# Performance work log

Measured on AMD Instinct MI355X. Metric: run time of the kernel, lower is better.

The kernel has to match this reference:

```python
import jax, jax.numpy as jnp
import numpy as np

B, C, H, W = 4, 128, 96, 96
INTER = C // 2


def setup_inputs() -> dict:
    key = jax.random.key(0)
    ks = jax.random.split(key, 6)
    scale = 1.0 / np.sqrt(C)
    return {
        "x1": jax.random.normal(ks[0], (B, C, H, W), dtype=jnp.float32),
        "x2": jax.random.normal(ks[1], (B, C, H, W), dtype=jnp.float32),
        "w_theta": jax.random.normal(ks[2], (INTER, C), dtype=jnp.float32) * scale,
        "w_phi": jax.random.normal(ks[3], (INTER, C), dtype=jnp.float32) * scale,
        "w_g": jax.random.normal(ks[4], (INTER, C), dtype=jnp.float32) * scale,
        "w_mask": jax.random.normal(ks[5], (C, INTER), dtype=jnp.float32) * (1.0 / np.sqrt(INTER)),
    }


def reference(x1, x2, w_theta, w_phi, w_g, w_mask):
    b, c, h1, w1 = x1.shape  # c == full channel
    inter = c // 2
    # 1x1 convs (no bias) == channel GEMMs
    theta = jnp.einsum('ic,bchw->bihw', w_theta, x1)   # [b, inter, h1, w1]
    phi   = jnp.einsum('ic,bchw->bihw', w_phi,   x2)   # [b, inter, h2, w2]
    g     = jnp.einsum('ic,bchw->bihw', w_g,     x2)   # [b, inter, h2, w2]
    # Faithful to original: .view(b, c, -1) with c = FULL channel count,
    # so the flattened length is H*W/2 and the contraction dim is c (row-major reshape).
    theta = theta.reshape(b, c, -1).transpose(0, 2, 1)  # [b, N1, c], N1 = h1*w1//2
    phi = phi.reshape(b, c, -1)                         # [b, c, N2]
    g = g.reshape(b, c, -1).transpose(0, 2, 1)          # [b, N2, c]
    scores = jnp.einsum('bnc,bcm->bnm', theta, phi)     # [b, N1, N2]
    attn = jax.nn.softmax(scores, axis=1)               # softmax over dim=1 (query axis!)
    y = jnp.einsum('bnm,bmc->bnc', attn, g)             # [b, N1, c]
    y = y.transpose(0, 2, 1).reshape(b, inter, h1, w1)  # [b, inter, h1, w1]
    mask = jnp.einsum('ci,bihw->bchw', w_mask, y)       # [b, c, h1, w1]
    return mask + x1
```

## Files before the change

kernel.cpp:

```cpp
#include <hip/hip_runtime.h>

typedef __attribute__((ext_vector_type(8))) short short8;
typedef __attribute__((ext_vector_type(4))) float f32x4;
typedef __attribute__((ext_vector_type(16))) float f32x16;
typedef unsigned short u16;
typedef unsigned int u32;

#define NB 4
#define CH 128
#define INTER2 64
#define HW2 9216
#define NN 4608
#define NSLICE 16
#define SLW2 288
#define PCH 136
#define APITCH 136

#if __has_builtin(__builtin_amdgcn_exp2f)
#define EXP2F __builtin_amdgcn_exp2f
#else
#define EXP2F exp2f
#endif

__device__ __forceinline__ u16 f2bf(float f) {
  u32 u = __float_as_uint(f);
  u += 0x7fffu + ((u >> 16) & 1u);
  return (u16)(u >> 16);
}
__device__ __forceinline__ float bf2f(u16 h) { return __uint_as_float(((u32)h) << 16); }
__device__ __forceinline__ u32 cvtpk(float lo, float hi) {
  u32 r;
  asm("v_cvt_pk_bf16_f32 %0, %1, %2" : "=v"(r) : "v"(lo), "v"(hi));
  return r;
}
__device__ __forceinline__ void gl_lds16(const u16* g, u16* l) {
  __builtin_amdgcn_global_load_lds(
      (const __attribute__((address_space(1))) unsigned int*)g,
      (__attribute__((address_space(3))) unsigned int*)l, 16, 0, 0);
}

__global__ void k_wcvt(const float* __restrict__ wt, const float* __restrict__ wp,
                       const float* __restrict__ wg, const float* __restrict__ wm,
                       u16* __restrict__ wtb, u16* __restrict__ wpb,
                       u16* __restrict__ wgb, u16* __restrict__ wmb) {
  int i = blockIdx.x * 256 + threadIdx.x;
  if (i < CH * INTER2) {
    wtb[i] = f2bf(wt[i]);
    wpb[i] = f2bf(wp[i]);
    wgb[i] = f2bf(wg[i]);
    wmb[i] = f2bf(wm[i]);
  }
}

__global__ __launch_bounds__(256) void k_conv(const float* __restrict__ x1,
                                              const float* __restrict__ x2,
                                              const u16* __restrict__ wtb,
                                              const u16* __restrict__ wpb,
                                              const u16* __restrict__ wgb,
                                              u16* __restrict__ Tt,
                                              u16* __restrict__ Pt,
                                              u16* __restrict__ Gn) {
  __shared__ u16 xT[64 * PCH];
  __shared__ u16 ot[64 * 72];
  const int tid = threadIdx.x;
  const int w = tid >> 6, l = tid & 63, lr = l & 15, lg = l >> 4;
  const int pt = blockIdx.x, b = blockIdx.y, z = blockIdx.z;
  const int p0 = pt * 64;
  const int h = (p0 >= NN) ? 1 : 0;
  const int n0 = p0 - h * NN;
  const float* X = (z ? x2 : x1) + (size_t)b * CH * HW2;

  {
    const int pq = (l & 15) * 4;
    const int cs = w + 4 * (l >> 4);
#pragma unroll
    for (int it = 0; it < 8; it++) {
      const int c = it * 16 + cs;
      float4 v = *(const float4*)(X + (size_t)c * HW2 + p0 + pq);
      xT[(pq + 0) * PCH + c] = f2bf(v.x);
      xT[(pq + 1) * PCH + c] = f2bf(v.y);
      xT[(pq + 2) * PCH + c] = f2bf(v.z);
      xT[(pq + 3) * PCH + c] = f2bf(v.w);
    }
  }
  short8 wsP[4], wsG[4];
  {
    const u16* W1 = z ? wpb : wtb;
#pragma unroll
    for (int ks = 0; ks < 4; ks++)
      wsP[ks] = *(const short8*)(W1 + (w * 16 + lr) * CH + ks * 32 + lg * 8);
    if (z) {
#pragma unroll
      for (int ks = 0; ks < 4; ks++)
        wsG[ks] = *(const short8*)(wgb + (w * 16 + lr) * CH + ks * 32 + lg * 8);
    }
  }
  __syncthreads();
  short8 xf[4][4];
#pragma unroll
  for (int tp = 0; tp < 4; tp++)
#pragma unroll
    for (int ks = 0; ks < 4; ks++)
      xf[tp][ks] = *(const short8*)(&xT[(tp * 16 + lr) * PCH + ks * 32 + lg * 8]);

  f32x4 accP[4];
#pragma unroll
  for (int tp = 0; tp < 4; tp++) {
#pragma unroll
    for (int j = 0; j < 4; j++) accP[tp][j] = 0.f;
#pragma unroll
    for (int ks = 0; ks < 4; ks++)
      accP[tp] = __builtin_amdgcn_mfma_f32_16x16x32_bf16(xf[tp][ks], wsP[ks], accP[tp], 0, 0, 0);
  }
#pragma unroll
  for (int tp = 0; tp < 4; tp++) {
#pragma unroll
    for (int j = 0; j < 4; j++)
      ot[(tp * 16 + lg * 4 + j) * 72 + w * 16 + lr] = f2bf(accP[tp][j]);
  }
  if (z) {
    f32x4 accG[4];
#pragma unroll
    for (int tp = 0; tp < 4; tp++) {
#pragma unroll
      for (int j = 0; j < 4; j++) accG[tp][j] = 0.f;
#pragma unroll
      for (int ks = 0; ks < 4; ks++)
        accG[tp] = __builtin_amdgcn_mfma_f32_16x16x32_bf16(wsG[ks], xf[tp][ks], accG[tp], 0, 0, 0);
    }
    u16* Gb = Gn + (size_t)b * CH * NN;
#pragma unroll
    for (int tp = 0; tp < 4; tp++) {
#pragma unroll
      for (int j = 0; j < 4; j++) {
        const int ig = w * 16 + lg * 4 + j;
        Gb[(size_t)((h << 6) + ig) * NN + n0 + tp * 16 + lr] = f2bf(accG[tp][j]);
      }
    }
  }
  __syncthreads();
  {
    u16* dst = (z ? Pt : Tt) + (size_t)b * NN * CH;
#pragma unroll
    for (int q = 0; q < 2; q++) {
      const int idx = tid * 2 + q;
      const int p = idx >> 3, c8 = (idx & 7) * 8;
      uint4 v = *(const uint4*)(&ot[p * 72 + c8]);
      *(uint4*)(dst + (size_t)(n0 + p) * CH + h * 64 + c8) = v;
    }
  }
}

__global__ __launch_bounds__(256) void k_den(const u16* __restrict__ Tt,
                                             const u16* __restrict__ Pt,
                                             float* __restrict__ denp) {
  const int tid = threadIdx.x;
  const int w = tid >> 6, l = tid & 63, lm = l & 31, lh = l >> 5;
  const int s = blockIdx.x & 15, mt = blockIdx.x >> 4;
  const int b = blockIdx.y;
  const int m0 = mt * 256;
  const int nbase = s * SLW2;
  const u16* PtB = Pt + (size_t)b * NN * CH;
  const u16* TtB = Tt + (size_t)b * NN * CH;

  short8 bf[2][8];
#pragma unroll
  for (int ms = 0; ms < 2; ms++)
#pragma unroll
    for (int ks = 0; ks < 8; ks++)
      bf[ms][ks] = *(const short8*)(PtB + (size_t)(m0 + w * 64 + ms * 32 + lm) * CH + ks * 16 + lh * 8);

  float den0 = 0.f, den1 = 0.f;
  short8 ac[8], an[8];
#pragma unroll
  for (int ks = 0; ks < 8; ks++)
    ac[ks] = *(const short8*)(TtB + (size_t)(nbase + lm) * CH + ks * 16 + lh * 8);

  for (int it = 0; it < 9; it++) {
    if (it + 1 < 9) {
      const int nr = nbase + (it + 1) * 32 + lm;
#pragma unroll
      for (int ks = 0; ks < 8; ks++)
        an[ks] = *(const short8*)(TtB + (size_t)nr * CH + ks * 16 + lh * 8);
    }
    f32x16 a0, a1;
#pragma unroll
    for (int q = 0; q < 16; q++) { a0[q] = 0.f; a1[q] = 0.f; }
#pragma unroll
    for (int ks = 0; ks < 8; ks++) {
      a0 = __builtin_amdgcn_mfma_f32_32x32x16_bf16(ac[ks], bf[0][ks], a0, 0, 0, 0);
      a1 = __builtin_amdgcn_mfma_f32_32x32x16_bf16(ac[ks], bf[1][ks], a1, 0, 0, 0);
    }
#pragma unroll
    for (int q = 0; q < 16; q++) {
      den0 += EXP2F(__builtin_fmaf(a0[q], 1.44269504f, -57.70780163f));
      den1 += EXP2F(__builtin_fmaf(a1[q], 1.44269504f, -57.70780163f));
    }
    if (it + 1 < 9) {
#pragma unroll
      for (int ks = 0; ks < 8; ks++) ac[ks] = an[ks];
    }
  }
  den0 += __shfl_xor(den0, 32, 64);
  den1 += __shfl_xor(den1, 32, 64);
  if (l < 32) {
    float* dp = denp + (size_t)(s * NB + b) * NN + m0 + w * 64;
    dp[lm] = den0;
    dp[32 + lm] = den1;
  }
}

__global__ __launch_bounds__(256) void k_rdn(const float* __restrict__ denp,
                                             float* __restrict__ rdn) {
  const int i = blockIdx.x * 256 + threadIdx.x;
  const int b = i / NN, m = i % NN;
  float s = 0.f;
#pragma unroll
  for (int s2 = 0; s2 < NSLICE; s2++) s += denp[(size_t)(s2 * NB + b) * NN + m];
  rdn[i] = 1.0f / s;
}

__global__ __launch_bounds__(256) void k_att(const u16* __restrict__ Tt,
                                             const u16* __restrict__ Pt,
                                             const u16* __restrict__ Gn,
                                             const float* __restrict__ rdn,
                                             float* __restrict__ Yp) {
  __shared__ u16 TtS[128 * 128];
  __shared__ u16 Atile[128 * APITCH];
  const int tid = threadIdx.x;
  const int w = tid >> 6, l = tid & 63, lr = l & 15, lg = l >> 4;
  const int lm = l & 31, lh = l >> 5;
  const int x = blockIdx.x;
  const int xcd = x & 7, rr = x >> 3;
  const int nt = rr >> 1;
  const int c = xcd + 8 * (rr & 1);
  const int b = c >> 2, sk = c & 3;
  const int n0 = nt * 128;
  const int mbase = sk * 1152;
  const u16* TtB = Tt + ((size_t)b * NN + n0) * CH;
  const u16* PtB = Pt + (size_t)b * NN * CH;
  const u16* GnB = Gn + (size_t)b * CH * NN;
  const float* rdnB = rdn + b * NN;

#pragma unroll
  for (int it = 0; it < 8; it++) {
    const int i = it * 256 + tid;
    const int row = i >> 4, slot = i & 15;
    gl_lds16(TtB + (size_t)row * CH + ((slot ^ (row & 15)) * 8),
             &TtS[(it * 256 + w * 64) * 8]);
  }
  __syncthreads();

  const int wc = w >> 1, wn = w & 1;
  f32x4 acc[4][4];
#pragma unroll
  for (int fa = 0; fa < 4; fa++)
#pragma unroll
    for (int fb = 0; fb < 4; fb++)
#pragma unroll
      for (int j = 0; j < 4; j++) acc[fa][fb][j] = 0.f;

  for (int ch = 0; ch < 9; ch++) {
    const int mch = mbase + ch * 128;
    short8 bf[8];
#pragma unroll
    for (int ks = 0; ks < 8; ks++)
      bf[ks] = *(const short8*)(PtB + (size_t)(mch + w * 32 + lm) * CH + ks * 16 + lh * 8);
    const float rv = rdnB[mch + w * 32 + lm];
#pragma unroll
    for (int ns = 0; ns < 4; ns++) {
      short8 af[8];
#pragma unroll
      for (int ks = 0; ks < 8; ks++)
        af[ks] = *(const short8*)(&TtS[(ns * 32 + lm) * 128 + (((ks * 2 + lh) ^ (lm & 15)) * 8)]);
      f32x16 sa;
#pragma unroll
      for (int q = 0; q < 16; q++) sa[q] = 0.f;
#pragma unroll
      for (int ks = 0; ks < 8; ks++)
        sa = __builtin_amdgcn_mfma_f32_32x32x16_bf16(af[ks], bf[ks], sa, 0, 0, 0);
#pragma unroll
      for (int q = 0; q < 16; q += 2) {
        const int nl = ns * 32 + (q & 3) + 8 * (q >> 2) + 4 * lh;
        float e0 = EXP2F(__builtin_fmaf(sa[q], 1.44269504f, -57.70780163f)) * rv;
        float e1 = EXP2F(__builtin_fmaf(sa[q + 1], 1.44269504f, -57.70780163f)) * rv;
        u32 pk = cvtpk(e0, e1);
        Atile[nl * APITCH + w * 32 + lm] = (u16)pk;
        Atile[(nl + 1) * APITCH + w * 32 + lm] = (u16)(pk >> 16);
      }
    }
    short8 gfc[4], gfn2[4];
#pragma unroll
    for (int fa = 0; fa < 4; fa++)
      gfc[fa] = *(const short8*)(GnB + (size_t)(wc * 64 + fa * 16 + lr) * NN + mch + lg * 8);
    __syncthreads();
#pragma unroll
    for (int ks = 0; ks < 4; ks++) {
      if (ks + 1 < 4) {
#pragma unroll
        for (int fa = 0; fa < 4; fa++)
          gfn2[fa] = *(const short8*)(GnB + (size_t)(wc * 64 + fa * 16 + lr) * NN + mch + (ks + 1) * 32 + lg * 8);
      }
      short8 pb[4];
#pragma unroll
      for (int fb = 0; fb < 4; fb++)
        pb[fb] = *(const short8*)(&Atile[(wn * 64 + fb * 16 + lr) * APITCH + ks * 32 + lg * 8]);
#pragma unroll
      for (int fa = 0; fa < 4; fa++)
#pragma unroll
        for (int fb = 0; fb < 4; fb++)
          acc[fa][fb] = __builtin_amdgcn_mfma_f32_16x16x32_bf16(gfc[fa], pb[fb], acc[fa][fb], 0, 0, 0);
      if (ks + 1 < 4) {
#pragma unroll
        for (int fa = 0; fa < 4; fa++) gfc[fa] = gfn2[fa];
      }
    }
    __syncthreads();
  }
  float* Yb = Yp + (size_t)(sk * NB + b) * CH * NN;
#pragma unroll
  for (int fa = 0; fa < 4; fa++) {
#pragma unroll
    for (int fb = 0; fb < 4; fb++) {
      const int n = n0 + wn * 64 + fb * 16 + lr;
#pragma unroll
      for (int j = 0; j < 4; j++) {
        const int d = wc * 64 + fa * 16 + lg * 4 + j;
        Yb[(size_t)d * NN + n] = acc[fa][fb][j];
      }
    }
  }
}

__global__ __launch_bounds__(256) void k_out(const float* __restrict__ Yp,
                                             const u16* __restrict__ wmb,
                                             const float* __restrict__ x1,
                                             float* __restrict__ out) {
  __shared__ u16 yy[64][72];
  const int tid = threadIdx.x;
  const int w = tid >> 6, l = tid & 63, lr = l & 15, lg = l >> 4;
  const int b = blockIdx.y;
  const int n0 = blockIdx.x * 32;
  const int nl = tid & 31, cch = tid >> 5;

  float v[16];
#pragma unroll
  for (int q = 0; q < 16; q++) v[q] = 0.f;
#pragma unroll
  for (int s2 = 0; s2 < 4; s2++) {
    const float* base = Yp + ((size_t)(s2 * NB + b) * CH + cch * 16) * NN + n0 + nl;
#pragma unroll
    for (int q = 0; q < 16; q++) v[q] += base[(size_t)q * NN];
  }
#pragma unroll
  for (int q = 0; q < 16; q++) {
    const int d = cch * 16 + q;
    yy[(d >> 6) * 32 + nl][d & 63] = f2bf(v[q]);
  }
  __syncthreads();

  const int wm3 = w >> 1, wp3 = w & 1;
  f32x4 eacc[4][2];
#pragma unroll
  for (int fa = 0; fa < 4; fa++)
#pragma unroll
    for (int fb = 0; fb < 2; fb++)
#pragma unroll
      for (int j = 0; j < 4; j++) eacc[fa][fb][j] = 0.f;
#pragma unroll
  for (int ks = 0; ks < 2; ks++) {
    short8 wa[4];
#pragma unroll
    for (int fa = 0; fa < 4; fa++)
      wa[fa] = *(const short8*)(wmb + (wm3 * 64 + fa * 16 + lr) * 64 + ks * 32 + lg * 8);
    short8 yb[2];
#pragma unroll
    for (int fb = 0; fb < 2; fb++)
      yb[fb] = *(const short8*)(&yy[wp3 * 32 + fb * 16 + lr][ks * 32 + lg * 8]);
#pragma unroll
    for (int fa = 0; fa < 4; fa++)
#pragma unroll
      for (int fb = 0; fb < 2; fb++)
        eacc[fa][fb] = __builtin_amdgcn_mfma_f32_16x16x32_bf16(wa[fa], yb[fb], eacc[fa][fb], 0, 0, 0);
  }
  const float* x1b = x1 + (size_t)b * CH * HW2;
  float* ob = out + (size_t)b * CH * HW2;
#pragma unroll
  for (int fa = 0; fa < 4; fa++) {
#pragma unroll
    for (int fb = 0; fb < 2; fb++) {
      const int pl = wp3 * 32 + fb * 16 + lr;
      const int col = n0 + (pl & 31) + (pl >> 5) * NN;
#pragma unroll
      for (int j = 0; j < 4; j++) {
        const int c = wm3 * 64 + fa * 16 + lg * 4 + j;
        const size_t o = (size_t)c * HW2 + col;
        ob[o] = eacc[fa][fb][j] + x1b[o];
      }
    }
  }
}

extern "C" void kernel_launch(void* const* d_in, const int* in_sizes, int n_in,
                              void* d_out, int out_size, void* d_ws, size_t ws_size,
                              hipStream_t stream) {
  const float* x1 = (const float*)d_in[0];
  const float* x2 = (const float*)d_in[1];
  const float* wt = (const float*)d_in[2];
  const float* wp = (const float*)d_in[3];
  const float* wg = (const float*)d_in[4];
  const float* wm = (const float*)d_in[5];
  float* out = (float*)d_out;

  char* ws = (char*)d_ws;
  const size_t SZ_T = (size_t)NB * NN * CH * 2;
  u16* Tt = (u16*)ws; ws += SZ_T;
  u16* Pt = (u16*)ws; ws += SZ_T;
  u16* Gn = (u16*)ws; ws += SZ_T;
  float* denp = (float*)ws; ws += (size_t)NSLICE * NB * NN * 4;
  float* rdn = (float*)ws; ws += (size_t)NB * NN * 4;
  u16* wtb = (u16*)ws; ws += (size_t)CH * INTER2 * 2;
  u16* wpb = (u16*)ws; ws += (size_t)CH * INTER2 * 2;
  u16* wgb = (u16*)ws; ws += (size_t)CH * INTER2 * 2;
  u16* wmb = (u16*)ws; ws += (size_t)CH * INTER2 * 2;
  float* Yp = (float*)ws; ws += (size_t)16 * CH * NN * 4;
  if (ws_size < (size_t)(ws - (char*)d_ws)) return;

  hipLaunchKernelGGL(k_wcvt, dim3(32), dim3(256), 0, stream, wt, wp, wg, wm, wtb, wpb, wgb, wmb);
  hipLaunchKernelGGL(k_conv, dim3(144, NB, 2), dim3(256), 0, stream, x1, x2, wtb, wpb, wgb, Tt, Pt, Gn);
  hipLaunchKernelGGL(k_den, dim3(288, NB), dim3(256), 0, stream, Tt, Pt, denp);
  hipLaunchKernelGGL(k_rdn, dim3(72), dim3(256), 0, stream, denp, rdn);
  hipLaunchKernelGGL(k_att, dim3(576), dim3(256), 0, stream, Tt, Pt, Gn, rdn, Yp);
  hipLaunchKernelGGL(k_out, dim3(144, NB), dim3(256), 0, stream, Yp, wmb, x1, out);
}
```

Measured before the change: 181.4 us.

## Double-buffer attention tile and software-pipeline score and PV stages

The attention kernel now works in 64-wide key chunks and keeps two LDS attention tiles. Each iteration runs the PV MFMAs for the previous chunk, at raised wave priority, alongside the QK and exp for the current chunk. This cuts the number of barriers per iteration from two to one. The aim is to overlap exp and LDS-write latency with matrix work, at the cost of twice as many loop iterations and a smaller per-chunk PV GEMM.

```diff
diff --git a/kernel.cpp b/kernel.cpp
--- a/kernel.cpp
+++ b/kernel.cpp
@@ -14,7 +14,6 @@
 #define NSLICE 16
 #define SLW2 288
 #define PCH 136
-#define APITCH 136
 
 #if __has_builtin(__builtin_amdgcn_exp2f)
 #define EXP2F __builtin_amdgcn_exp2f
@@ -226,7 +225,7 @@
                                              const float* __restrict__ rdn,
                                              float* __restrict__ Yp) {
   __shared__ u16 TtS[128 * 128];
-  __shared__ u16 Atile[128 * APITCH];
+  __shared__ u16 Atile[2][128 * 72];
   const int tid = threadIdx.x;
   const int w = tid >> 6, l = tid & 63, lr = l & 15, lg = l >> 4;
   const int lm = l & 31, lh = l >> 5;
@@ -249,8 +248,8 @@
     gl_lds16(TtB + (size_t)row * CH + ((slot ^ (row & 15)) * 8),
              &TtS[(it * 256 + w * 64) * 8]);
   }
-  __syncthreads();
-
+
+  const int wm2 = w & 1, wn2 = w >> 1;
   const int wc = w >> 1, wn = w & 1;
   f32x4 acc[4][4];
 #pragma unroll
@@ -260,59 +259,60 @@
 #pragma unroll
       for (int j = 0; j < 4; j++) acc[fa][fb][j] = 0.f;
 
-  for (int ch = 0; ch < 9; ch++) {
-    const int mch = mbase + ch * 128;
-    short8 bf[8];
-#pragma unroll
-    for (int ks = 0; ks < 8; ks++)
-      bf[ks] = *(const short8*)(PtB + (size_t)(mch + w * 32 + lm) * CH + ks * 16 + lh * 8);
-    const float rv = rdnB[mch + w * 32 + lm];
-#pragma unroll
-    for (int ns = 0; ns < 4; ns++) {
-      short8 af[8];
+  __syncthreads();
+
+  for (int ch = 0; ch < 19; ch++) {
+    if (ch >= 1) {
+      const int mp = mbase + (ch - 1) * 64;
+      const u16* Ab = &Atile[(ch - 1) & 1][0];
+      __builtin_amdgcn_s_setprio(1);
+#pragma unroll
+      for (int ks = 0; ks < 2; ks++) {
+        short8 gf[4], pb[4];
+#pragma unroll
+        for (int fa = 0; fa < 4; fa++)
+          gf[fa] = *(const short8*)(GnB + (size_t)(wc * 64 + fa * 16 + lr) * NN + mp + ks * 32 + lg * 8);
+#pragma unroll
+        for (int fb = 0; fb < 4; fb++)
+          pb[fb] = *(const short8*)(Ab + (wn * 64 + fb * 16 + lr) * 72 + ks * 32 + lg * 8);
+#pragma unroll
+        for (int fa = 0; fa < 4; fa++)
+#pragma unroll
+          for (int fb = 0; fb < 4; fb++)
+            acc[fa][fb] = __builtin_amdgcn_mfma_f32_16x16x32_bf16(gf[fa], pb[fb], acc[fa][fb], 0, 0, 0);
+      }
+      __builtin_amdgcn_s_setprio(0);
+    }
+    if (ch < 18) {
+      const int mch = mbase + ch * 64;
+      u16* Aw = &Atile[ch & 1][0];
+      short8 bf[8];
 #pragma unroll
       for (int ks = 0; ks < 8; ks++)
-        af[ks] = *(const short8*)(&TtS[(ns * 32 + lm) * 128 + (((ks * 2 + lh) ^ (lm & 15)) * 8)]);
-      f32x16 sa;
-#pragma unroll
-      for (int q = 0; q < 16; q++) sa[q] = 0.f;
-#pragma unroll
-      for (int ks = 0; ks < 8; ks++)
-        sa = __builtin_amdgcn_mfma_f32_32x32x16_bf16(af[ks], bf[ks], sa, 0, 0, 0);
-#pragma unroll
-      for (int q = 0; q < 16; q += 2) {
-        const int nl = ns * 32 + (q & 3) + 8 * (q >> 2) + 4 * lh;
-        float e0 = EXP2F(__builtin_fmaf(sa[q], 1.44269504f, -57.70780163f)) * rv;
-        float e1 = EXP2F(__builtin_fmaf(sa[q + 1], 1.44269504f, -57.70780163f)) * rv;
-        u32 pk = cvtpk(e0, e1);
-        Atile[nl * APITCH + w * 32 + lm] = (u16)pk;
-        Atile[(nl + 1) * APITCH + w * 32 + lm] = (u16)(pk >> 16);
-      }
-    }
-    short8 gfc[4], gfn2[4];
-#pragma unroll
-    for (int fa = 0; fa < 4; fa++)
-      gfc[fa] = *(const short8*)(GnB + (size_t)(wc * 64 + fa * 16 + lr) * NN + mch + lg * 8);
-    __syncthreads();
-#pragma unroll
-    for (int ks = 0; ks < 4; ks++) {
-      if (ks + 1 < 4) {
-#pragma unroll
-        for (int fa = 0; fa < 4; fa++)
-          gfn2[fa] = *(const short8*)(GnB + (size_t)(wc * 64 + fa * 16 + lr) * NN + mch + (ks + 1) * 32 + lg * 8);
-      }
-      short8 pb[4];
-#pragma unroll
-      for (int fb = 0; fb < 4; fb++)
-        pb[fb] = *(const short8*)(&Atile[(wn * 64 + fb * 16 + lr) * APITCH + ks * 32 + lg * 8]);
-#pragma unroll
-      for (int fa = 0; fa < 4; fa++)
-#pragma unroll
-        for (int fb = 0; fb < 4; fb++)
-          acc[fa][fb] = __builtin_amdgcn_mfma_f32_16x16x32_bf16(gfc[fa], pb[fb], acc[fa][fb], 0, 0, 0);
-      if (ks + 1 < 4) {
-#pragma unroll
-        for (int fa = 0; fa < 4; fa++) gfc[fa] = gfn2[fa];
+        bf[ks] = *(const short8*)(PtB + (size_t)(mch + wm2 * 32 + lm) * CH + ks * 16 + lh * 8);
+      const float rv = rdnB[mch + wm2 * 32 + lm];
+#pragma unroll
+      for (int ns = 0; ns < 2; ns++) {
+        const int nrow = wn2 * 64 + ns * 32 + lm;
+        short8 af[8];
+#pragma unroll
+        for (int ks = 0; ks < 8; ks++)
+          af[ks] = *(const short8*)(&TtS[nrow * 128 + (((ks * 2 + lh) ^ (lm & 15)) * 8)]);
+        f32x16 sa;
+#pragma unroll
+        for (int q = 0; q < 16; q++) sa[q] = 0.f;
+#pragma unroll
+        for (int ks = 0; ks < 8; ks++)
+          sa = __builtin_amdgcn_mfma_f32_32x32x16_bf16(af[ks], bf[ks], sa, 0, 0, 0);
+#pragma unroll
+        for (int q = 0; q < 16; q += 2) {
+          const int nl = wn2 * 64 + ns * 32 + (q & 3) + 8 * (q >> 2) + 4 * lh;
+          float e0 = EXP2F(__builtin_fmaf(sa[q], 1.44269504f, -57.70780163f)) * rv;
+          float e1 = EXP2F(__builtin_fmaf(sa[q + 1], 1.44269504f, -57.70780163f)) * rv;
+          u32 pk = cvtpk(e0, e1);
+          Aw[nl * 72 + wm2 * 32 + lm] = (u16)pk;
+          Aw[(nl + 1) * 72 + wm2 * 32 + lm] = (u16)(pk >> 16);
+        }
       }
     }
     __syncthreads();
```

New measurement: 219.2 us. +20.9%, slower.
